# Kernel optimization log

Hardware: AMD Instinct MI355X
Metric: run time of the kernel (lower is better)

Reference implementation:

```python
import jax, jax.numpy as jnp
import numpy as np

NUM_INPUTS, NUM_HIDDEN, NUM_OUTPUTS = 512, 1024, 35
T, B = 100, 512
N_HID_LAYERS = 4  # number of hidden Leaky layers (num_layers)
SLOPE = 25.0      # snntorch surrogate.fast_sigmoid default slope
BETA, THR = 0.95, 1.0


@jax.custom_vjp
def spike(x):
    # Heaviside forward, fast-sigmoid surrogate backward
    return (x > 0).astype(x.dtype)

def _spike_fwd(x):
    return (x > 0).astype(x.dtype), x

def _spike_bwd(x, g):
    return (g / (SLOPE * jnp.abs(x) + 1.0) ** 2,)

spike.defvjp(_spike_fwd, _spike_bwd)


def leaky(x, mem, beta, thr):
    # snntorch Leaky, reset_mechanism='subtract':
    # reset computed from PREVIOUS mem (detached), then decay+input, then fire
    reset = jax.lax.stop_gradient((mem - thr > 0).astype(x.dtype))
    mem = jnp.clip(beta, 0.0, 1.0) * mem + x - reset * thr
    spk = spike(mem - thr)
    return spk, mem


def setup_inputs() -> dict:
    key = jax.random.key(0)
    ks = jax.random.split(key, 8)
    data = jax.random.normal(ks[0], (T, B, NUM_INPUTS), dtype=jnp.float32)
    s_in = 1.0 / np.sqrt(NUM_INPUTS)
    s_h = 1.0 / np.sqrt(NUM_HIDDEN)
    W_in = jax.random.uniform(ks[1], (NUM_HIDDEN, NUM_INPUTS), minval=-s_in, maxval=s_in, dtype=jnp.float32)
    b_in = jax.random.uniform(ks[2], (NUM_HIDDEN,), minval=-s_in, maxval=s_in, dtype=jnp.float32)
    W_h = jax.random.uniform(ks[3], (N_HID_LAYERS - 1, NUM_HIDDEN, NUM_HIDDEN), minval=-s_h, maxval=s_h, dtype=jnp.float32)
    b_h = jax.random.uniform(ks[4], (N_HID_LAYERS - 1, NUM_HIDDEN), minval=-s_h, maxval=s_h, dtype=jnp.float32)
    W_out = jax.random.uniform(ks[5], (NUM_OUTPUTS, NUM_HIDDEN), minval=-s_h, maxval=s_h, dtype=jnp.float32)
    b_out = jax.random.uniform(ks[6], (NUM_OUTPUTS,), minval=-s_h, maxval=s_h, dtype=jnp.float32)
    # learn_beta/learn_threshold: each Leaky holds its own (identically initialized) params
    beta_h = jnp.full((N_HID_LAYERS, NUM_HIDDEN), BETA, dtype=jnp.float32)
    thr_h = jnp.full((N_HID_LAYERS, NUM_HIDDEN), THR, dtype=jnp.float32)
    beta_o = jnp.full((NUM_OUTPUTS,), BETA, dtype=jnp.float32)
    thr_o = jnp.full((NUM_OUTPUTS,), THR, dtype=jnp.float32)
    return {"data": data, "W_in": W_in, "b_in": b_in, "W_h": W_h, "b_h": b_h,
            "W_out": W_out, "b_out": b_out, "beta_h": beta_h, "thr_h": thr_h,
            "beta_o": beta_o, "thr_o": thr_o, "timestep": 100}


def reference(data, W_in, b_in, W_h, b_h, W_out, b_out, beta_h, thr_h, beta_o, thr_o, timestep):
    n_hid = beta_h.shape[0]
    Bsz = data.shape[1]

    def step(mems, x_t):
        new_mems = []
        x = x_t @ W_in.T + b_in
        x, m = leaky(x, mems[0], beta_h[0], thr_h[0])
        new_mems.append(m)
        for i in range(n_hid - 1):
            z = x @ W_h[i].T + b_h[i]
            x, m = leaky(z, mems[i + 1], beta_h[i + 1], thr_h[i + 1])
            new_mems.append(m)
        z = x @ W_out.T + b_out
        spk, m = leaky(z, mems[n_hid], beta_o, thr_o)
        new_mems.append(m)
        return tuple(new_mems), spk

    mems0 = tuple([jnp.zeros((Bsz, NUM_HIDDEN), dtype=data.dtype) for _ in range(n_hid)]
                  + [jnp.zeros((Bsz, NUM_OUTPUTS), dtype=data.dtype)])
    _, spk_rec = jax.lax.scan(step, mems0, data[:timestep])
    return spk_rec  # [T, B, num_outputs]
```

## Files before the change

### kernel.cpp

```cpp
#include <hip/hip_runtime.h>
#include <hip/hip_bf16.h>


#define NB 512
#define NH 1024
#define NI 512
#define NO 35
#define TT 100
#define NT 8
#define BITFRAME 16384

typedef __bf16 bf16x8 __attribute__((ext_vector_type(8)));
typedef float f32x4 __attribute__((ext_vector_type(4)));
typedef int   i32x4 __attribute__((ext_vector_type(4)));

__device__ __forceinline__ size_t tiled_off(int row, int k, int KT) {
    return ((size_t)((row >> 4) * KT + (k >> 5)) * 64
            + (row & 15) + (((k >> 3) & 3) << 4)) * 8 + (k & 7);
}

__device__ __forceinline__ void leaky_upd(float zin, float mprev, float be, float th,
                                          float& mnew, float& spk) {
    float rs = (mprev - th > 0.0f) ? th : 0.0f;
    float bc = fminf(fmaxf(be, 0.0f), 1.0f);
    mnew = bc * mprev + zin - rs;
    spk  = (mnew - th > 0.0f) ? 1.0f : 0.0f;
}

#define WS_MEM123   0u
#define WS_MEM0     6291456u
#define WS_MEMO     8388608u
#define WS_FLAGS    8486912u
#define WS_GEN      8487936u
#define WS_RING0    8488192u
#define WS_RING1    9536768u
#define WS_RING2    10585344u
#define WS_RING3    11633920u
#define WS_W8       12682496u
#define WS_WIT      25265408u
#define WS_WOT      28411136u
#define WS_Z0       28706048u
#define STEP_BYTES  2097152u

__global__ __launch_bounds__(256)
void split_weights_i8(const float* __restrict__ W_h, signed char* __restrict__ W8) {
    const int id = blockIdx.x * 256 + threadIdx.x;
    const int layer = id >> 16;
    const int rem = id & 65535;
    const int n = rem >> 6;
    const int k0 = (rem & 63) << 4;
    const float* src = W_h + ((size_t)layer * NH + n) * NH + k0;
    const int kq = k0 >> 4;
    const int ck = kq >> 2;
    const int lane = (n & 15) | ((kq & 3) << 4);
    signed char* dstL = W8 + (size_t)layer * 4 * NH * NH;
    const size_t gb = ((size_t)(n >> 4) * 16 + ck) * 1024 + lane * 16;

    signed char q1[16], q2[16], q3[16], q4[16];
    #pragma unroll
    for (int j = 0; j < 16; ++j) {
        float w = src[j];
        float f1 = rintf(w * 0x1p11f);   float r1 = w  - f1 * 0x1p-11f;
        float f2 = rintf(r1 * 0x1p18f);  float r2 = r1 - f2 * 0x1p-18f;
        float f3 = rintf(r2 * 0x1p25f);  float r3 = r2 - f3 * 0x1p-25f;
        float f4 = rintf(r3 * 0x1p32f);
        q1[j] = (signed char)(int)f1; q2[j] = (signed char)(int)f2;
        q3[j] = (signed char)(int)f3; q4[j] = (signed char)(int)f4;
    }
    #pragma unroll
    for (int j = 0; j < 16; ++j) {
        dstL[(size_t)0 * 64 * 16384 + gb + j] = q1[j];
        dstL[(size_t)1 * 64 * 16384 + gb + j] = q2[j];
        dstL[(size_t)2 * 64 * 16384 + gb + j] = q3[j];
        dstL[(size_t)3 * 64 * 16384 + gb + j] = q4[j];
    }
}

__global__ __launch_bounds__(256)
void split_win(const float* __restrict__ W_in, __bf16* __restrict__ Wi_t) {
    const int id = blockIdx.x * 256 + threadIdx.x;
    const int n = id >> 6;
    const int k0 = (id & 63) << 3;
    const float* src = W_in + (size_t)n * NI + k0;
    const size_t PS = (size_t)NH * NI;
    const size_t off = tiled_off(n, k0, 16);
    bf16x8 p1, p2, p3;
    #pragma unroll
    for (int j = 0; j < 8; ++j) {
        float w = src[j];
        __bf16 a = (__bf16)w;  float r1 = w - (float)a;
        __bf16 b = (__bf16)r1; float r2 = r1 - (float)b;
        __bf16 c = (__bf16)r2;
        p1[j] = a; p2[j] = b; p3[j] = c;
    }
    *reinterpret_cast<bf16x8*>(Wi_t + 0 * PS + off) = p1;
    *reinterpret_cast<bf16x8*>(Wi_t + 1 * PS + off) = p2;
    *reinterpret_cast<bf16x8*>(Wi_t + 2 * PS + off) = p3;
}

__global__ __launch_bounds__(256)
void split_wout(const float* __restrict__ W_out, __bf16* __restrict__ Wo_t) {
    const int id = blockIdx.x * 256 + threadIdx.x;
    if (id >= 48 * 128) return;
    const int o = id >> 7;
    const int k0 = (id & 127) << 3;
    const size_t PS = (size_t)48 * NH;
    const size_t off = tiled_off(o, k0, 32);
    bf16x8 p1 = {}, p2 = {}, p3 = {};
    if (o < NO) {
        const float* src = W_out + (size_t)o * NH + k0;
        #pragma unroll
        for (int j = 0; j < 8; ++j) {
            float w = src[j];
            __bf16 a = (__bf16)w;  float r1 = w - (float)a;
            __bf16 b = (__bf16)r1; float r2 = r1 - (float)b;
            __bf16 c = (__bf16)r2;
            p1[j] = a; p2[j] = b; p3[j] = c;
        }
    }
    *reinterpret_cast<bf16x8*>(Wo_t + 0 * PS + off) = p1;
    *reinterpret_cast<bf16x8*>(Wo_t + 1 * PS + off) = p2;
    *reinterpret_cast<bf16x8*>(Wo_t + 2 * PS + off) = p3;
}

__global__ __launch_bounds__(256)
void z0_gemm(const float* __restrict__ X,
             const __bf16* __restrict__ Wi_t,
             const float* __restrict__ bias,
             float* __restrict__ Z0)
{
    const int tid = threadIdx.x;
    const int lane = tid & 63;
    const int w = tid >> 6;
    const int wm = w >> 1, wn = w & 1;
    const int m_base = blockIdx.y * 64 + wm * 32;
    const int n_base = blockIdx.x * 128 + wn * 64;
    const size_t PS = (size_t)NH * NI;

    f32x4 acc[2][4] = {};
    const float* asrc[2];
    #pragma unroll
    for (int mt = 0; mt < 2; ++mt)
        asrc[mt] = X + (size_t)(m_base + mt * 16 + (lane & 15)) * NI + ((lane >> 4) << 3);

    float4 c0[2], c1[2];
    #pragma unroll
    for (int mt = 0; mt < 2; ++mt) {
        c0[mt] = *reinterpret_cast<const float4*>(asrc[mt]);
        c1[mt] = *reinterpret_cast<const float4*>(asrc[mt] + 4);
    }

    for (int kt = 0; kt < 16; ++kt) {
        float4 n0[2], n1[2];
        if (kt < 15) {
            #pragma unroll
            for (int mt = 0; mt < 2; ++mt) {
                n0[mt] = *reinterpret_cast<const float4*>(asrc[mt] + (kt + 1) * 32);
                n1[mt] = *reinterpret_cast<const float4*>(asrc[mt] + (kt + 1) * 32 + 4);
            }
        }
        bf16x8 a1[2], a2[2], a3[2];
        #pragma unroll
        for (int mt = 0; mt < 2; ++mt) {
            float xv[8] = {c0[mt].x, c0[mt].y, c0[mt].z, c0[mt].w,
                           c1[mt].x, c1[mt].y, c1[mt].z, c1[mt].w};
            #pragma unroll
            for (int j = 0; j < 8; ++j) {
                float x = xv[j];
                __bf16 h1 = (__bf16)x;  float r1 = x - (float)h1;
                __bf16 h2 = (__bf16)r1; float r2 = r1 - (float)h2;
                __bf16 h3 = (__bf16)r2;
                a1[mt][j] = h1; a2[mt][j] = h2; a3[mt][j] = h3;
            }
        }
        #pragma unroll
        for (int nt = 0; nt < 4; ++nt) {
            const size_t bo = ((size_t)(((n_base >> 4) + nt) * 16 + kt) * 64 + lane) * 8;
            bf16x8 b1 = *reinterpret_cast<const bf16x8*>(Wi_t + bo);
            bf16x8 b2 = *reinterpret_cast<const bf16x8*>(Wi_t + PS + bo);
            bf16x8 b3 = *reinterpret_cast<const bf16x8*>(Wi_t + 2 * PS + bo);
            #pragma unroll
            for (int mt = 0; mt < 2; ++mt) {
                f32x4 A = acc[mt][nt];
                A = __builtin_amdgcn_mfma_f32_16x16x32_bf16(a1[mt], b1, A, 0, 0, 0);
                A = __builtin_amdgcn_mfma_f32_16x16x32_bf16(a1[mt], b2, A, 0, 0, 0);
                A = __builtin_amdgcn_mfma_f32_16x16x32_bf16(a2[mt], b1, A, 0, 0, 0);
                A = __builtin_amdgcn_mfma_f32_16x16x32_bf16(a2[mt], b2, A, 0, 0, 0);
                A = __builtin_amdgcn_mfma_f32_16x16x32_bf16(a1[mt], b3, A, 0, 0, 0);
                A = __builtin_amdgcn_mfma_f32_16x16x32_bf16(a3[mt], b1, A, 0, 0, 0);
                acc[mt][nt] = A;
            }
        }
        if (kt < 15) {
            #pragma unroll
            for (int mt = 0; mt < 2; ++mt) { c0[mt] = n0[mt]; c1[mt] = n1[mt]; }
        }
    }

    const int c = lane & 15;
    const int r0 = (lane >> 4) * 4;
    #pragma unroll
    for (int nt = 0; nt < 4; ++nt) {
        const int n = n_base + nt * 16 + c;
        const float bi = bias[n];
        #pragma unroll
        for (int mt = 0; mt < 2; ++mt) {
            #pragma unroll
            for (int r = 0; r < 4; ++r) {
                const int m = m_base + mt * 16 + r0 + r;
                const int tl = m >> 9, b = m & 511;
                Z0[(size_t)tl * (NB * NH) + tiled_off(b, n, 32)] = acc[mt][nt][r] + bi;
            }
        }
    }
}

__device__ __forceinline__ void gridbar(int* flags, int* gen, int target) {
    __syncthreads();
    if (threadIdx.x == 0) {
        __builtin_amdgcn_fence(__ATOMIC_RELEASE, "agent");
        __hip_atomic_store(&flags[blockIdx.x], target, __ATOMIC_RELAXED, __HIP_MEMORY_SCOPE_AGENT);
    }
    if (blockIdx.x == 0) {
        if (threadIdx.x < 64) {
            const int l = threadIdx.x;
            for (;;) {
                int v0 = __hip_atomic_load(&flags[l],       __ATOMIC_RELAXED, __HIP_MEMORY_SCOPE_AGENT);
                int v1 = __hip_atomic_load(&flags[l + 64],  __ATOMIC_RELAXED, __HIP_MEMORY_SCOPE_AGENT);
                int v2 = __hip_atomic_load(&flags[l + 128], __ATOMIC_RELAXED, __HIP_MEMORY_SCOPE_AGENT);
                int v3 = __hip_atomic_load(&flags[l + 192], __ATOMIC_RELAXED, __HIP_MEMORY_SCOPE_AGENT);
                int mn = min(min(v0, v1), min(v2, v3));
                if (__all(mn >= target)) break;
                __builtin_amdgcn_s_sleep(1);
            }
        }
        __syncthreads();
        if (threadIdx.x == 0) {
            __builtin_amdgcn_fence(__ATOMIC_ACQ_REL, "agent");
            __hip_atomic_store(gen, target, __ATOMIC_RELAXED, __HIP_MEMORY_SCOPE_AGENT);
        }
    } else if (threadIdx.x == 0) {
        while (__hip_atomic_load(gen, __ATOMIC_RELAXED, __HIP_MEMORY_SCOPE_AGENT) < target)
            __builtin_amdgcn_s_sleep(2);
    }
    __syncthreads();
    __builtin_amdgcn_fence(__ATOMIC_ACQUIRE, "agent");
}

template<int NS>
__device__ __forceinline__ void hidden_run_i8(
    const unsigned int* const* Xp, unsigned short* const* Yp,
    const signed char* Wl, int cs, int rh, int w, int lane, int ckoff,
    float (&memr)[2][2][4], const float (&bi)[2], const float (&be)[2],
    const float (&th)[2])
{
    const int row  = lane & 15;
    const int lg   = lane >> 4;
    const int wsel = lg >> 1;
    const int hsel = (lg & 1) * 16;

    i32x4 acc[NS][2][2][4] = {};

    unsigned int bw[NS][2];
    #pragma unroll
    for (int q = 0; q < NS; ++q)
        #pragma unroll
        for (int i = 0; i < 2; ++i)
            bw[q][i] = Xp[q][((rh * 16 + w * 2 + i) * 32 + ckoff * 2 + wsel) * 16 + row];

    i32x4 bf[8];
    #pragma unroll
    for (int pn = 0; pn < 8; ++pn)
        bf[pn] = *reinterpret_cast<const i32x4*>(Wl + pn * 16384 + ckoff * 1024 + lane * 16);

    for (int ckk = 0; ckk < 16; ++ckk) {
        const int ck = (ckk + ckoff) & 15;
        const int ckn = (ck + 1) & 15;
        unsigned int nb[NS][2];
        i32x4 nf[8];
        if (ckk < 15) {
            #pragma unroll
            for (int pn = 0; pn < 8; ++pn)
                nf[pn] = *reinterpret_cast<const i32x4*>(
                    Wl + pn * 16384 + ckn * 1024 + lane * 16);
            #pragma unroll
            for (int q = 0; q < NS; ++q)
                #pragma unroll
                for (int i = 0; i < 2; ++i)
                    nb[q][i] = Xp[q][((rh * 16 + w * 2 + i) * 32 + ckn * 2 + wsel) * 16 + row];
        }

        __builtin_amdgcn_s_setprio(1);
        #pragma unroll
        for (int q = 0; q < NS; ++q) {
            #pragma unroll
            for (int i = 0; i < 2; ++i) {
                unsigned int half = (bw[q][i] >> hsel) & 0xFFFFu;
                union { unsigned int u[4]; i32x4 v; } a;
                a.u[0] = (((half      ) & 0xFu) * 0x204081u) & 0x01010101u;
                a.u[1] = (((half >>  4) & 0xFu) * 0x204081u) & 0x01010101u;
                a.u[2] = (((half >>  8) & 0xFu) * 0x204081u) & 0x01010101u;
                a.u[3] = (((half >> 12) & 0xFu) * 0x204081u) & 0x01010101u;
                #pragma unroll
                for (int nt = 0; nt < 2; ++nt)
                    #pragma unroll
                    for (int p = 0; p < 4; ++p)
                        acc[q][i][nt][p] = __builtin_amdgcn_mfma_i32_16x16x64_i8(
                            a.v, bf[p * 2 + nt], acc[q][i][nt][p], 0, 0, 0);
            }
        }
        __builtin_amdgcn_s_setprio(0);

        if (ckk < 15) {
            #pragma unroll
            for (int q = 0; q < NS; ++q) { bw[q][0] = nb[q][0]; bw[q][1] = nb[q][1]; }
            #pragma unroll
            for (int pn = 0; pn < 8; ++pn) bf[pn] = nf[pn];
        }
    }

    #pragma unroll
    for (int q = 0; q < NS; ++q) {
        #pragma unroll
        for (int i = 0; i < 2; ++i) {
            #pragma unroll
            for (int nt = 0; nt < 2; ++nt) {
                #pragma unroll
                for (int r = 0; r < 4; ++r) {
                    float z = (float)acc[q][i][nt][3][r] * 0x1p-32f
                            + (float)acc[q][i][nt][2][r] * 0x1p-25f;
                    z += (float)acc[q][i][nt][1][r] * 0x1p-18f;
                    z += (float)acc[q][i][nt][0][r] * 0x1p-11f;
                    float mn, sp;
                    leaky_upd(z + bi[nt], memr[i][nt][r], be[nt], th[nt], mn, sp);
                    memr[i][nt][r] = mn;
                    unsigned long long bal = __ballot(sp != 0.0f);
                    if ((lane & 15) == 0) {
                        const int rr = (lane >> 4) * 4 + r;
                        Yp[q][(((rh * 16 + w * 2 + i) * 32 + cs) * 16 + rr) * 2 + nt] =
                            (unsigned short)((bal >> ((lane >> 4) * 16)) & 0xFFFFu);
                    }
                }
            }
        }
    }
}

__global__ __launch_bounds__(512, 1)
void snn_pipe(const float* __restrict__ Z0,
              const signed char* __restrict__ W8,
              const __bf16* __restrict__ Wo_t,
              const float* __restrict__ b_h,
              const float* __restrict__ b_out,
              const float* __restrict__ beta_h,
              const float* __restrict__ thr_h,
              const float* __restrict__ beta_o,
              const float* __restrict__ thr_o,
              float* __restrict__ mem123,
              float* __restrict__ mem0_g,
              float* __restrict__ memo_g,
              unsigned int* __restrict__ ring0, unsigned int* __restrict__ ring1,
              unsigned int* __restrict__ ring2, unsigned int* __restrict__ ring3,
              float* __restrict__ out,
              int* __restrict__ flags, int* __restrict__ gen,
              int t0, int tc)
{
    __shared__ signed char Wl[8 * 16 * 1024];
    __shared__ unsigned long long lut[16];

    const int blk  = blockIdx.x;
    const int tid  = threadIdx.x;
    const int lane = tid & 63;
    const int w    = tid >> 6;

    if (tid < 16) {
        unsigned int lo = ((tid & 1) ? 0x3F80u : 0u) | ((tid & 2) ? 0x3F800000u : 0u);
        unsigned int hi = ((tid & 4) ? 0x3F80u : 0u) | ((tid & 8) ? 0x3F800000u : 0u);
        lut[tid] = ((unsigned long long)hi << 32) | lo;
    }

    const int G = (tc + NT - 1) / NT;

    if (blk < 192) {
        const int ell = blk >> 6;
        const int cs  = (blk & 63) >> 1;
        const int rh  = blk & 1;
        const int ckoff = (w >> 2) * 8;
        {
            const signed char* Wsrc = W8 + (size_t)ell * 4 * NH * NH;
            for (int idx = tid; idx < 8 * 1024; idx += 512) {
                const int pn = idx >> 10, off = idx & 1023;
                const int p = pn >> 1, nt = pn & 1;
                *reinterpret_cast<int4*>(Wl + pn * 16384 + off * 16) =
                    *reinterpret_cast<const int4*>(
                        Wsrc + (size_t)(p * 64 + cs * 2 + nt) * 16384 + off * 16);
            }
        }

        const int c = lane & 15;
        const int r0v = (lane >> 4) * 4;
        float* memg = mem123 + (size_t)ell * (NB * NH);
        float bi[2], be[2], th[2];
        #pragma unroll
        for (int nt = 0; nt < 2; ++nt) {
            const int n = cs * 32 + nt * 16 + c;
            bi[nt] = b_h[ell * NH + n];
            be[nt] = beta_h[(ell + 1) * NH + n];
            th[nt] = thr_h[(ell + 1) * NH + n];
        }
        float memr[2][2][4];
        #pragma unroll
        for (int i = 0; i < 2; ++i)
            #pragma unroll
            for (int nt = 0; nt < 2; ++nt)
                #pragma unroll
                for (int r = 0; r < 4; ++r)
                    memr[i][nt][r] = memg[(size_t)(rh * 256 + (w * 2 + i) * 16 + r0v + r) * NH
                                          + cs * 32 + nt * 16 + c];

        const unsigned int* rin = (ell == 0) ? ring0 : (ell == 1) ? ring1 : ring2;
        unsigned int* rout      = (ell == 0) ? ring1 : (ell == 1) ? ring2 : ring3;

        __syncthreads();

        for (int p = 0; p < G + 4; ++p) {
            const int g = p - 1 - ell;
            if (g >= 0 && g < G) {
                const int sbase = g * NT;
                const int send  = (sbase + NT < tc) ? sbase + NT : tc;
                const int slot0 = (g & 1) * NT;
                int s = sbase;
                while (s < send) {
                    const int base = slot0 + (s - sbase);
                    const unsigned int* Xp[2];
                    unsigned short* Yp[2];
                    if (send - s >= 2) {
                        #pragma unroll
                        for (int q = 0; q < 2; ++q) {
                            Xp[q] = rin + (size_t)(base + q) * BITFRAME;
                            Yp[q] = (unsigned short*)(rout + (size_t)(base + q) * BITFRAME);
                        }
                        hidden_run_i8<2>(Xp, Yp, Wl, cs, rh, w, lane, ckoff, memr, bi, be, th);
                        s += 2;
                    } else {
                        Xp[0] = rin + (size_t)base * BITFRAME;
                        Yp[0] = (unsigned short*)(rout + (size_t)base * BITFRAME);
                        hidden_run_i8<1>(Xp, Yp, Wl, cs, rh, w, lane, ckoff, memr, bi, be, th);
                        s += 1;
                    }
                }
            }
            gridbar(flags, gen, p + 1);
        }

        #pragma unroll
        for (int i = 0; i < 2; ++i)
            #pragma unroll
            for (int nt = 0; nt < 2; ++nt)
                #pragma unroll
                for (int r = 0; r < 4; ++r)
                    memg[(size_t)(rh * 256 + (w * 2 + i) * 16 + r0v + r) * NH
                         + cs * 32 + nt * 16 + c] = memr[i][nt][r];
    } else if (blk < 224) {
        const bool outw = (w < 3);
        const int omt = blk - 192;
        const int ont = w;
        const int c = lane & 15, r0v = (lane >> 4) * 4;
        const int row = lane & 15, sh2 = (lane >> 4) * 8;
        const int oo = ont * 16 + c;
        const size_t OPS = (size_t)48 * NH;
        float mo[4] = {0.f, 0.f, 0.f, 0.f};
        float obi = 0.f, obe = 0.f, oth = 1.f;
        if (outw && oo < NO) {
            obi = b_out[oo]; obe = beta_o[oo]; oth = thr_o[oo];
            #pragma unroll
            for (int r = 0; r < 4; ++r) mo[r] = memo_g[(omt * 16 + r0v + r) * NO + oo];
        }
        __syncthreads();

        for (int p = 0; p < G + 4; ++p) {
            if (outw) {
                const int go = p - 4;
                if (go >= 0 && go < G) {
                    const int sbase = go * NT;
                    const int send  = (sbase + NT < tc) ? sbase + NT : tc;
                    const int slot0 = (go & 1) * NT;
                    for (int s = sbase; s < send; ++s) {
                        const unsigned int* Xw =
                            ring3 + (size_t)(slot0 + s - sbase) * BITFRAME;
                        f32x4 acc = {};
                        for (int kt = 0; kt < 32; ++kt) {
                            unsigned int by = (Xw[(omt * 32 + kt) * 16 + row] >> sh2) & 0xffu;
                            union { unsigned long long u[2]; bf16x8 v; } a;
                            a.u[0] = lut[by & 15u];
                            a.u[1] = lut[by >> 4];
                            const size_t bo = ((size_t)(ont * 32 + kt) * 64 + lane) * 8;
                            bf16x8 q1 = *reinterpret_cast<const bf16x8*>(Wo_t + bo);
                            bf16x8 q2 = *reinterpret_cast<const bf16x8*>(Wo_t + OPS + bo);
                            bf16x8 q3 = *reinterpret_cast<const bf16x8*>(Wo_t + 2 * OPS + bo);
                            acc = __builtin_amdgcn_mfma_f32_16x16x32_bf16(a.v, q1, acc, 0, 0, 0);
                            acc = __builtin_amdgcn_mfma_f32_16x16x32_bf16(a.v, q2, acc, 0, 0, 0);
                            acc = __builtin_amdgcn_mfma_f32_16x16x32_bf16(a.v, q3, acc, 0, 0, 0);
                        }
                        if (oo < NO) {
                            #pragma unroll
                            for (int r = 0; r < 4; ++r) {
                                float mn, sp;
                                leaky_upd(acc[r] + obi, mo[r], obe, oth, mn, sp);
                                mo[r] = mn;
                                out[((size_t)(t0 + s) * NB + omt * 16 + r0v + r) * NO + oo] = sp;
                            }
                        }
                    }
                }
            }
            gridbar(flags, gen, p + 1);
        }

        if (outw && oo < NO) {
            #pragma unroll
            for (int r = 0; r < 4; ++r) memo_g[(omt * 16 + r0v + r) * NO + oo] = mo[r];
        }
    } else {
        const int wi   = (blk - 224) * 512 + tid;
        const int mtb  = wi >> 9;
        const int ktb  = (wi >> 4) & 31;
        const int i0   = (mtb * 32 + ktb) * 512 + (wi & 15) * 8;

        float m0[32], be0[32], th0[32];
        #pragma unroll
        for (int byt = 0; byt < 4; ++byt)
            #pragma unroll
            for (int j = 0; j < 8; ++j) {
                m0[byt * 8 + j]  = mem0_g[i0 + byt * 128 + j];
                be0[byt * 8 + j] = beta_h[ktb * 32 + byt * 8 + j];
                th0[byt * 8 + j] = thr_h[ktb * 32 + byt * 8 + j];
            }
        __syncthreads();

        for (int p = 0; p < G + 4; ++p) {
            if (p < G) {
                const int sbase = p * NT;
                const int send  = (sbase + NT < tc) ? sbase + NT : tc;
                const int slot0 = (p & 1) * NT;
                for (int s = sbase; s < send; ++s) {
                    const float* zs = Z0 + (size_t)s * (NB * NH) + i0;
                    float4 zv[8];
                    #pragma unroll
                    for (int byt = 0; byt < 4; ++byt) {
                        zv[byt * 2]     = *reinterpret_cast<const float4*>(zs + byt * 128);
                        zv[byt * 2 + 1] = *reinterpret_cast<const float4*>(zs + byt * 128 + 4);
                    }
                    unsigned int bits = 0;
                    #pragma unroll
                    for (int e = 0; e < 32; ++e) {
                        float z = reinterpret_cast<const float*>(zv)[e];
                        float mn, sp;
                        leaky_upd(z, m0[e], be0[e], th0[e], mn, sp);
                        m0[e] = mn;
                        bits |= (sp != 0.0f ? 1u : 0u) << e;
                    }
                    ring0[(size_t)(slot0 + s - sbase) * BITFRAME + wi] = bits;
                }
            }
            gridbar(flags, gen, p + 1);
        }

        #pragma unroll
        for (int byt = 0; byt < 4; ++byt)
            #pragma unroll
            for (int j = 0; j < 8; ++j)
                mem0_g[i0 + byt * 128 + j] = m0[byt * 8 + j];
    }
}

extern "C" void kernel_launch(void* const* d_in, const int* in_sizes, int n_in,
                              void* d_out, int out_size, void* d_ws, size_t ws_size,
                              hipStream_t stream) {
    const float* data   = (const float*)d_in[0];
    const float* W_in   = (const float*)d_in[1];
    const float* b_in   = (const float*)d_in[2];
    const float* W_h    = (const float*)d_in[3];
    const float* b_h    = (const float*)d_in[4];
    const float* W_out  = (const float*)d_in[5];
    const float* b_out  = (const float*)d_in[6];
    const float* beta_h = (const float*)d_in[7];
    const float* thr_h  = (const float*)d_in[8];
    const float* beta_o = (const float*)d_in[9];
    const float* thr_o  = (const float*)d_in[10];
    float* out = (float*)d_out;

    char* ws = (char*)d_ws;
    float*        mem123 = (float*)(ws + WS_MEM123);
    float*        mem0_g = (float*)(ws + WS_MEM0);
    float*        memo_g = (float*)(ws + WS_MEMO);
    int*          flags  = (int*)(ws + WS_FLAGS);
    int*          gen    = (int*)(ws + WS_GEN);
    unsigned int* ring0  = (unsigned int*)(ws + WS_RING0);
    unsigned int* ring1  = (unsigned int*)(ws + WS_RING1);
    unsigned int* ring2  = (unsigned int*)(ws + WS_RING2);
    unsigned int* ring3  = (unsigned int*)(ws + WS_RING3);
    signed char*  W8     = (signed char*)(ws + WS_W8);
    __bf16*       Wi_t   = (__bf16*)(ws + WS_WIT);
    __bf16*       Wo_t   = (__bf16*)(ws + WS_WOT);
    float*        Z0     = (float*)(ws + WS_Z0);

    size_t avail = (ws_size > WS_Z0) ? (ws_size - WS_Z0) / STEP_BYTES : 1;
    int Tc = (int)(avail < 1 ? 1 : (avail > TT ? TT : avail));

    hipMemsetAsync(ws, 0, WS_RING0, stream);
    split_weights_i8<<<dim3(768), dim3(256), 0, stream>>>(W_h, W8);
    split_win<<<dim3(256), dim3(256), 0, stream>>>(W_in, Wi_t);
    split_wout<<<dim3(24), dim3(256), 0, stream>>>(W_out, Wo_t);

    for (int t0c = 0; t0c < TT; t0c += Tc) {
        const int tcc = (TT - t0c < Tc) ? (TT - t0c) : Tc;
        z0_gemm<<<dim3(NH / 128, tcc * (NB / 64)), dim3(256), 0, stream>>>(
            data + (size_t)t0c * NB * NI, Wi_t, b_in, Z0);
        hipMemsetAsync(ws + WS_FLAGS, 0, 1280, stream);
        snn_pipe<<<dim3(256), dim3(512), 0, stream>>>(
            Z0, W8, Wo_t, b_h, b_out, beta_h, thr_h, beta_o, thr_o,
            mem123, mem0_g, memo_g, ring0, ring1, ring2, ring3, out,
            flags, gen, t0c, tcc);
    }
}
```

Before: 1.495 ms.

## Double persistent block to 1024 threads, one row tile per wave

The persistent pipeline kernel now launches 1024 threads per block. In the hidden-layer blocks each of the 16 waves owns a single 16-row M tile instead of two, which halves accumulator and membrane registers per wave. The register double-buffered prefetch of LDS weight fragments is dropped: fragments are now loaded from LDS at each K chunk, with start offsets staggered across waves. The layer-0 blocks leave the extra 512 threads idle apart from the grid barrier. The aim is more waves per CU to hide latency, at the cost of twice the total LDS weight reads and less per-wave reuse of each weight fragment.

```diff
diff --git a/kernel.cpp b/kernel.cpp
--- a/kernel.cpp
+++ b/kernel.cpp
@@ -250,8 +250,8 @@
 template<int NS>
 __device__ __forceinline__ void hidden_run_i8(
     const unsigned int* const* Xp, unsigned short* const* Yp,
-    const signed char* Wl, int cs, int rh, int w, int lane, int ckoff,
-    float (&memr)[2][2][4], const float (&bi)[2], const float (&be)[2],
+    const signed char* Wl, int cs, int mt16, int lane, int ckoff,
+    float (&memr)[2][4], const float (&bi)[2], const float (&be)[2],
     const float (&th)[2])
 {
     const int row  = lane & 15;
@@ -259,94 +259,76 @@
     const int wsel = lg >> 1;
     const int hsel = (lg & 1) * 16;
 
-    i32x4 acc[NS][2][2][4] = {};
-
-    unsigned int bw[NS][2];
+    i32x4 acc[NS][2][4] = {};
+
+    unsigned int bw[NS];
     #pragma unroll
     for (int q = 0; q < NS; ++q)
-        #pragma unroll
-        for (int i = 0; i < 2; ++i)
-            bw[q][i] = Xp[q][((rh * 16 + w * 2 + i) * 32 + ckoff * 2 + wsel) * 16 + row];
-
-    i32x4 bf[8];
-    #pragma unroll
-    for (int pn = 0; pn < 8; ++pn)
-        bf[pn] = *reinterpret_cast<const i32x4*>(Wl + pn * 16384 + ckoff * 1024 + lane * 16);
+        bw[q] = Xp[q][(mt16 * 32 + ckoff * 2 + wsel) * 16 + row];
 
     for (int ckk = 0; ckk < 16; ++ckk) {
-        const int ck = (ckk + ckoff) & 15;
+        const int ck  = (ckk + ckoff) & 15;
         const int ckn = (ck + 1) & 15;
-        unsigned int nb[NS][2];
-        i32x4 nf[8];
+        unsigned int nb[NS];
         if (ckk < 15) {
             #pragma unroll
-            for (int pn = 0; pn < 8; ++pn)
-                nf[pn] = *reinterpret_cast<const i32x4*>(
-                    Wl + pn * 16384 + ckn * 1024 + lane * 16);
-            #pragma unroll
             for (int q = 0; q < NS; ++q)
+                nb[q] = Xp[q][(mt16 * 32 + ckn * 2 + wsel) * 16 + row];
+        }
+        i32x4 bf[8];
+        #pragma unroll
+        for (int pn = 0; pn < 8; ++pn)
+            bf[pn] = *reinterpret_cast<const i32x4*>(Wl + pn * 16384 + ck * 1024 + lane * 16);
+
+        __builtin_amdgcn_s_setprio(1);
+        #pragma unroll
+        for (int q = 0; q < NS; ++q) {
+            unsigned int half = (bw[q] >> hsel) & 0xFFFFu;
+            union { unsigned int u[4]; i32x4 v; } a;
+            a.u[0] = (((half      ) & 0xFu) * 0x204081u) & 0x01010101u;
+            a.u[1] = (((half >>  4) & 0xFu) * 0x204081u) & 0x01010101u;
+            a.u[2] = (((half >>  8) & 0xFu) * 0x204081u) & 0x01010101u;
+            a.u[3] = (((half >> 12) & 0xFu) * 0x204081u) & 0x01010101u;
+            #pragma unroll
+            for (int nt = 0; nt < 2; ++nt)
                 #pragma unroll
-                for (int i = 0; i < 2; ++i)
-                    nb[q][i] = Xp[q][((rh * 16 + w * 2 + i) * 32 + ckn * 2 + wsel) * 16 + row];
-        }
-
-        __builtin_amdgcn_s_setprio(1);
-        #pragma unroll
-        for (int q = 0; q < NS; ++q) {
-            #pragma unroll
-            for (int i = 0; i < 2; ++i) {
-                unsigned int half = (bw[q][i] >> hsel) & 0xFFFFu;
-                union { unsigned int u[4]; i32x4 v; } a;
-                a.u[0] = (((half      ) & 0xFu) * 0x204081u) & 0x01010101u;
-                a.u[1] = (((half >>  4) & 0xFu) * 0x204081u) & 0x01010101u;
-                a.u[2] = (((half >>  8) & 0xFu) * 0x204081u) & 0x01010101u;
-                a.u[3] = (((half >> 12) & 0xFu) * 0x204081u) & 0x01010101u;
-                #pragma unroll
-                for (int nt = 0; nt < 2; ++nt)
-                    #pragma unroll
-                    for (int p = 0; p < 4; ++p)
-                        acc[q][i][nt][p] = __builtin_amdgcn_mfma_i32_16x16x64_i8(
-                            a.v, bf[p * 2 + nt], acc[q][i][nt][p], 0, 0, 0);
-            }
+                for (int p = 0; p < 4; ++p)
+                    acc[q][nt][p] = __builtin_amdgcn_mfma_i32_16x16x64_i8(
+                        a.v, bf[p * 2 + nt], acc[q][nt][p], 0, 0, 0);
         }
         __builtin_amdgcn_s_setprio(0);
 
         if (ckk < 15) {
             #pragma unroll
-            for (int q = 0; q < NS; ++q) { bw[q][0] = nb[q][0]; bw[q][1] = nb[q][1]; }
-            #pragma unroll
-            for (int pn = 0; pn < 8; ++pn) bf[pn] = nf[pn];
+            for (int q = 0; q < NS; ++q) bw[q] = nb[q];
         }
     }
 
     #pragma unroll
     for (int q = 0; q < NS; ++q) {
         #pragma unroll
-        for (int i = 0; i < 2; ++i) {
-            #pragma unroll
-            for (int nt = 0; nt < 2; ++nt) {
-                #pragma unroll
-                for (int r = 0; r < 4; ++r) {
-                    float z = (float)acc[q][i][nt][3][r] * 0x1p-32f
-                            + (float)acc[q][i][nt][2][r] * 0x1p-25f;
-                    z += (float)acc[q][i][nt][1][r] * 0x1p-18f;
-                    z += (float)acc[q][i][nt][0][r] * 0x1p-11f;
-                    float mn, sp;
-                    leaky_upd(z + bi[nt], memr[i][nt][r], be[nt], th[nt], mn, sp);
-                    memr[i][nt][r] = mn;
-                    unsigned long long bal = __ballot(sp != 0.0f);
-                    if ((lane & 15) == 0) {
-                        const int rr = (lane >> 4) * 4 + r;
-                        Yp[q][(((rh * 16 + w * 2 + i) * 32 + cs) * 16 + rr) * 2 + nt] =
-                            (unsigned short)((bal >> ((lane >> 4) * 16)) & 0xFFFFu);
-                    }
+        for (int nt = 0; nt < 2; ++nt) {
+            #pragma unroll
+            for (int r = 0; r < 4; ++r) {
+                float z = (float)acc[q][nt][3][r] * 0x1p-32f
+                        + (float)acc[q][nt][2][r] * 0x1p-25f;
+                z += (float)acc[q][nt][1][r] * 0x1p-18f;
+                z += (float)acc[q][nt][0][r] * 0x1p-11f;
+                float mn, sp;
+                leaky_upd(z + bi[nt], memr[nt][r], be[nt], th[nt], mn, sp);
+                memr[nt][r] = mn;
+                unsigned long long bal = __ballot(sp != 0.0f);
+                if ((lane & 15) == 0) {
+                    const int rr = (lane >> 4) * 4 + r;
+                    Yp[q][((mt16 * 32 + cs) * 16 + rr) * 2 + nt] =
+                        (unsigned short)((bal >> ((lane >> 4) * 16)) & 0xFFFFu);
                 }
             }
         }
     }
 }
 
-__global__ __launch_bounds__(512, 1)
+__global__ __launch_bounds__(1024, 1)
 void snn_pipe(const float* __restrict__ Z0,
               const signed char* __restrict__ W8,
               const __bf16* __restrict__ Wo_t,
@@ -385,10 +367,11 @@
         const int ell = blk >> 6;
         const int cs  = (blk & 63) >> 1;
         const int rh  = blk & 1;
-        const int ckoff = (w >> 2) * 8;
+        const int mt16 = rh * 16 + w;
+        const int ckoff = ((w >> 2) & 3) * 4;
         {
             const signed char* Wsrc = W8 + (size_t)ell * 4 * NH * NH;
-            for (int idx = tid; idx < 8 * 1024; idx += 512) {
+            for (int idx = tid; idx < 8 * 1024; idx += 1024) {
                 const int pn = idx >> 10, off = idx & 1023;
                 const int p = pn >> 1, nt = pn & 1;
                 *reinterpret_cast<int4*>(Wl + pn * 16384 + off * 16) =
@@ -408,15 +391,13 @@
             be[nt] = beta_h[(ell + 1) * NH + n];
             th[nt] = thr_h[(ell + 1) * NH + n];
         }
-        float memr[2][2][4];
-        #pragma unroll
-        for (int i = 0; i < 2; ++i)
-            #pragma unroll
-            for (int nt = 0; nt < 2; ++nt)
-                #pragma unroll
-                for (int r = 0; r < 4; ++r)
-                    memr[i][nt][r] = memg[(size_t)(rh * 256 + (w * 2 + i) * 16 + r0v + r) * NH
-                                          + cs * 32 + nt * 16 + c];
+        float memr[2][4];
+        #pragma unroll
+        for (int nt = 0; nt < 2; ++nt)
+            #pragma unroll
+            for (int r = 0; r < 4; ++r)
+                memr[nt][r] = memg[(size_t)(mt16 * 16 + r0v + r) * NH
+                                   + cs * 32 + nt * 16 + c];
 
         const unsigned int* rin = (ell == 0) ? ring0 : (ell == 1) ? ring1 : ring2;
         unsigned int* rout      = (ell == 0) ? ring1 : (ell == 1) ? ring2 : ring3;
@@ -440,12 +421,12 @@
                             Xp[q] = rin + (size_t)(base + q) * BITFRAME;
                             Yp[q] = (unsigned short*)(rout + (size_t)(base + q) * BITFRAME);
                         }
-                        hidden_run_i8<2>(Xp, Yp, Wl, cs, rh, w, lane, ckoff, memr, bi, be, th);
+                        hidden_run_i8<2>(Xp, Yp, Wl, cs, mt16, lane, ckoff, memr, bi, be, th);
                         s += 2;
                     } else {
                         Xp[0] = rin + (size_t)base * BITFRAME;
                         Yp[0] = (unsigned short*)(rout + (size_t)base * BITFRAME);
-                        hidden_run_i8<1>(Xp, Yp, Wl, cs, rh, w, lane, ckoff, memr, bi, be, th);
+                        hidden_run_i8<1>(Xp, Yp, Wl, cs, mt16, lane, ckoff, memr, bi, be, th);
                         s += 1;
                     }
                 }
@@ -454,13 +435,11 @@
         }
 
         #pragma unroll
-        for (int i = 0; i < 2; ++i)
-            #pragma unroll
-            for (int nt = 0; nt < 2; ++nt)
-                #pragma unroll
-                for (int r = 0; r < 4; ++r)
-                    memg[(size_t)(rh * 256 + (w * 2 + i) * 16 + r0v + r) * NH
-                         + cs * 32 + nt * 16 + c] = memr[i][nt][r];
+        for (int nt = 0; nt < 2; ++nt)
+            #pragma unroll
+            for (int r = 0; r < 4; ++r)
+                memg[(size_t)(mt16 * 16 + r0v + r) * NH
+                     + cs * 32 + nt * 16 + c] = memr[nt][r];
     } else if (blk < 224) {
         const bool outw = (w < 3);
         const int omt = blk - 192;
@@ -522,24 +501,27 @@
             for (int r = 0; r < 4; ++r) memo_g[(omt * 16 + r0v + r) * NO + oo] = mo[r];
         }
     } else {
+        const bool act = (tid < 512);
         const int wi   = (blk - 224) * 512 + tid;
         const int mtb  = wi >> 9;
         const int ktb  = (wi >> 4) & 31;
         const int i0   = (mtb * 32 + ktb) * 512 + (wi & 15) * 8;
 
         float m0[32], be0[32], th0[32];
-        #pragma unroll
-        for (int byt = 0; byt < 4; ++byt)
-            #pragma unroll
-            for (int j = 0; j < 8; ++j) {
-                m0[byt * 8 + j]  = mem0_g[i0 + byt * 128 + j];
-                be0[byt * 8 + j] = beta_h[ktb * 32 + byt * 8 + j];
-                th0[byt * 8 + j] = thr_h[ktb * 32 + byt * 8 + j];
-            }
+        if (act) {
+            #pragma unroll
+            for (int byt = 0; byt < 4; ++byt)
+                #pragma unroll
+                for (int j = 0; j < 8; ++j) {
+                    m0[byt * 8 + j]  = mem0_g[i0 + byt * 128 + j];
+                    be0[byt * 8 + j] = beta_h[ktb * 32 + byt * 8 + j];
+                    th0[byt * 8 + j] = thr_h[ktb * 32 + byt * 8 + j];
+                }
+        }
         __syncthreads();
 
         for (int p = 0; p < G + 4; ++p) {
-            if (p < G) {
+            if (act && p < G) {
                 const int sbase = p * NT;
                 const int send  = (sbase + NT < tc) ? sbase + NT : tc;
                 const int slot0 = (p & 1) * NT;
@@ -566,11 +548,13 @@
             gridbar(flags, gen, p + 1);
         }
 
-        #pragma unroll
-        for (int byt = 0; byt < 4; ++byt)
-            #pragma unroll
-            for (int j = 0; j < 8; ++j)
-                mem0_g[i0 + byt * 128 + j] = m0[byt * 8 + j];
+        if (act) {
+            #pragma unroll
+            for (int byt = 0; byt < 4; ++byt)
+                #pragma unroll
+                for (int j = 0; j < 8; ++j)
+                    mem0_g[i0 + byt * 128 + j] = m0[byt * 8 + j];
+        }
     }
 }
 
@@ -618,7 +602,7 @@
         z0_gemm<<<dim3(NH / 128, tcc * (NB / 64)), dim3(256), 0, stream>>>(
             data + (size_t)t0c * NB * NI, Wi_t, b_in, Z0);
         hipMemsetAsync(ws + WS_FLAGS, 0, 1280, stream);
-        snn_pipe<<<dim3(256), dim3(512), 0, stream>>>(
+        snn_pipe<<<dim3(256), dim3(1024), 0, stream>>>(
             Z0, W8, Wo_t, b_h, b_out, beta_h, thr_h, beta_o, thr_o,
             mem123, mem0_g, memo_g, ring0, ring1, ring2, ring3, out,
             flags, gen, t0c, tcc);
```

Result: slower. 2.805 ms (+87.7%).
